# Optimization experiments

Hardware: AMD Instinct MI355X
Metric: run time of the kernel (lower is better)

## Reference

```python
import jax, jax.numpy as jnp
import numpy as np
import math

B, NH, DIM = 8, 12, 768
NP, NF = 196, 16            # n (patches per frame), num_frames
DH = DIM // NH              # 64
D3 = 3 * DH                 # per-head feature dim after projection (192)
SEQ = NP * NF               # 3136 body tokens (+1 cls)
ROT = DH                    # rotary dim (RotaryEmbedding(dim=64))
SCALE = 1.0 / (math.sqrt(DH) * NH)


def _heads(t):
    b, s, _ = t.shape
    return t.reshape(b, s, NH, D3).transpose(0, 2, 1, 3)  # b h s d


def _rope(x):
    # lucidrains-style interleaved rotary on the first ROT dims of each head
    s = x.shape[2]
    inv_freq = 1.0 / (10000.0 ** (jnp.arange(0, ROT, 2, dtype=jnp.float32) / ROT))
    freqs = jnp.arange(s, dtype=jnp.float32)[:, None] * inv_freq  # [s, ROT/2]
    freqs = jnp.repeat(freqs, 2, axis=-1)                          # [s, ROT]
    cos, sin = jnp.cos(freqs), jnp.sin(freqs)
    xr, xp = x[..., :ROT], x[..., ROT:]
    x1, x2 = xr[..., ::2], xr[..., 1::2]
    half = jnp.stack((-x2, x1), axis=-1).reshape(xr.shape)
    return jnp.concatenate([xr * cos + half * sin, xp], axis=-1)


def _att_sum(q, k, v):
    # softmax(q k^T * SCALE) v, then sum over queries keepdim (dim 2)
    p = jax.nn.softmax(jnp.einsum('bhqd,bhkd->bhqk', q, k) * SCALE, axis=-1)
    return jnp.einsum('bhqk,bhkd->bhqd', p, v).sum(axis=2, keepdims=True)


def setup_inputs():
    key = jax.random.key(0)
    ks = jax.random.split(key, 11)
    p = lambda k, sh: jax.random.normal(k, sh, jnp.float32) * 0.02
    return {
        'x': jax.random.normal(ks[0], (B, SEQ + 1, DIM), jnp.float32),
        'Wq': p(ks[1], (DIM, 3 * DIM)), 'bq': p(ks[2], (3 * DIM,)),
        'Wk': p(ks[3], (DIM, 3 * DIM)), 'bk': p(ks[4], (3 * DIM,)),
        'Wv': p(ks[5], (DIM, 3 * DIM)), 'bv': p(ks[6], (3 * DIM,)),
        'Wt': p(ks[7], (3 * DIM, DIM)), 'bt': p(ks[8], (DIM,)),
        'Wf': p(ks[9], (3 * DIM, DIM)), 'bf': p(ks[10], (DIM,)),
    }


def reference(x, Wq, bq, Wk, bk, Wv, bv, Wt, bt, Wf, bf):
    body = x[:, 1:, :]
    # NOTE: the original swaps k/v projections for body tokens (k_mat uses self.v, v_mat uses self.k)
    q = _rope(_heads(body @ Wq + bq))
    k = _rope(_heads(body @ Wv + bv))
    v = _heads(body @ Wk + bk)

    # cls-token attention over the full sequence (correct k/v mapping here)
    q_cls = _heads(x[:, 0:1, :] @ Wq + bq)          # [b,h,1,d]
    k_cls = _heads(x @ Wk + bk)
    v_cls = _heads(x @ Wv + bv)
    p_cls = jax.nn.softmax(jnp.einsum('bhqd,bhkd->bhqk', q_cls, k_cls) * SCALE, axis=-1)
    cls_out = jnp.einsum('bhqk,bhkd->bhqd', p_cls, v_cls)  # [b,h,1,d]

    # temporal attention per spatial position x = 1..NP-1, vectorized
    # token index t = f*NP + x  ->  reshape [b,h,NF,NP,d], move spatial first
    qg = q.reshape(B, NH, NF, NP, D3).transpose(0, 1, 3, 2, 4)[:, :, 1:]  # [b,h,NP-1,NF,d]
    kg = k.reshape(B, NH, NF, NP, D3).transpose(0, 1, 3, 2, 4)[:, :, 1:]
    vg = v.reshape(B, NH, NF, NP, D3).transpose(0, 1, 3, 2, 4)[:, :, 1:]
    pg = jax.nn.softmax(jnp.einsum('bhxfd,bhxgd->bhxfg', qg, kg) * SCALE, axis=-1)
    tmp = jnp.einsum('bhxfg,bhxgd->bhxfd', pg, vg).sum(axis=3)  # sum over query frames -> [b,h,NP-1,d]

    temporal = jnp.tile(tmp, (1, 1, NF, 1))  # torch .repeat tiles -> [b,h,(NP-1)*NF,d]
    ti = temporal.transpose(0, 2, 1, 3).reshape(B, (NP - 1) * NF, NH * D3) @ Wt + bt

    # second pass (q uses self.q, v uses self.k, k uses self.v per original)
    q2 = _heads(ti @ Wq + bq)
    v2 = _heads(ti @ Wk + bk)
    k2 = _heads(ti @ Wv + bv)
    outs = [_att_sum(q2[:, :, 0:NP], k2[:, :, 0:NP], v2[:, :, 0:NP])]
    for xi in range(1, NF):  # small fixed loop over frames
        outs.append(_att_sum(q2[:, :, xi:xi + NP], k2[:, :, xi::NP], v2[:, :, xi::NP]))
    t2 = jnp.concatenate(outs, axis=2)        # [b,h,NF,d]
    t2 = jnp.tile(t2, (1, 1, NP, 1))          # [b,h,SEQ,d]
    t2 = jnp.concatenate([cls_out, t2], axis=2)  # [b,h,SEQ+1,d]
    return t2.transpose(0, 2, 1, 3).reshape(B, SEQ + 1, NH * D3) @ Wf + bf
```

## Files before the change

kernel.cpp:

```cpp
#include <hip/hip_runtime.h>
#include <cstdint>
#include <cstddef>


typedef unsigned short u16;
typedef __attribute__((ext_vector_type(8))) short short8;
typedef __attribute__((ext_vector_type(4))) float f32x4;

#define DEV static __device__ __forceinline__
#define AS1 __attribute__((address_space(1)))
#define AS3 __attribute__((address_space(3)))

DEV float b2f(u16 u) { union { unsigned int i; float f; } v; v.i = ((unsigned int)u) << 16; return v.f; }
DEV float b2fs(short s) { return b2f((u16)s); }
DEV u16 f2b(float f) {
    union { float f; unsigned int i; } v; v.f = f;
    unsigned int r = v.i + 0x7fffu + ((v.i >> 16) & 1u);
    return (u16)(r >> 16);
}
DEV void gld16(const u16* g, u16* l) {
    __builtin_amdgcn_global_load_lds((AS1 void*)(g), (AS3 void*)(l), 16, 0, 0);
}

DEV int detect_fl(const u16* x) {
    int lane = threadIdx.x & 63;
    const u16* p = x + lane * 8;
    int c = 0;
#pragma unroll
    for (int j = 0; j < 8; j++) c += (((p[j] >> 7) & 0xFFu) >= 134u);
#pragma unroll
    for (int off = 32; off; off >>= 1) c += __shfl_xor(c, off);
    return c > 8;
}

constexpr int   ROWS  = 3137;
constexpr int   NPm1  = 195;
constexpr int   MT    = 8 * NPm1;
constexpr int   N3    = 2304;
constexpr float SCALE = 1.0f / 96.0f;
constexpr size_t P2Z  = (size_t)MT * N3;
constexpr int   CLS_NS = 32;
constexpr int   CLS_RS = 99;
constexpr int   LDK   = 200;

DEV float wave_max(float v) {
#pragma unroll
    for (int off = 32; off; off >>= 1) v = fmaxf(v, __shfl_xor(v, off));
    return v;
}
DEV float wave_sum(float v) {
#pragma unroll
    for (int off = 32; off; off >>= 1) v += __shfl_xor(v, off);
    return v;
}
DEV float block_max256(float v, float* red) {
    v = wave_max(v);
    __syncthreads();
    if ((threadIdx.x & 63) == 0) red[threadIdx.x >> 6] = v;
    __syncthreads();
    return fmaxf(fmaxf(red[0], red[1]), fmaxf(red[2], red[3]));
}
float __device__ __forceinline__ block_sum256(float v, float* red) {
    v = wave_sum(v);
    __syncthreads();
    if ((threadIdx.x & 63) == 0) red[threadIdx.x >> 6] = v;
    __syncthreads();
    return (red[0] + red[1]) + (red[2] + red[3]);
}

DEV void do_transpose(const void* in, u16* out, int R, int C,
                      int bx, int by, int fl, u16 (*tls)[33]) {
    int tx = threadIdx.x & 31, ty = threadIdx.x >> 5;
#pragma unroll
    for (int i = 0; i < 32; i += 8) {
        int r = by + ty + i, c = bx + tx;
        size_t idx = (size_t)r * C + c;
        tls[ty + i][tx] = fl ? f2b(((const float*)in)[idx]) : ((const u16*)in)[idx];
    }
    __syncthreads();
#pragma unroll
    for (int i = 0; i < 32; i += 8) {
        int c = bx + ty + i, r = by + tx;
        out[(size_t)c * R + r] = tls[tx][ty + i];
    }
}

__global__ __launch_bounds__(256) void prep(const u16* __restrict__ x,
                                            const void* __restrict__ Wq,
                                            const void* __restrict__ Wk,
                                            const void* __restrict__ Wv,
                                            const void* __restrict__ Wt,
                                            const void* __restrict__ Wf,
                                            const void* __restrict__ bq,
                                            const void* __restrict__ bk,
                                            const void* __restrict__ bv,
                                            u16* __restrict__ WT,
                                            u16* __restrict__ WtT,
                                            u16* __restrict__ WfT,
                                            u16* __restrict__ xb,
                                            float* __restrict__ wacc,
                                            float* __restrict__ ropeT,
                                            float* __restrict__ biasF,
                                            int usexb) {
    __shared__ u16 tls[32][33];
    int bid = blockIdx.x;
    if (bid < 5184) {
        int fl = detect_fl(x);
        int z = bid / 1728, t = bid % 1728;
        const void* W = (z == 0) ? Wq : (z == 1) ? Wk : Wv;
        do_transpose(W, WT + (size_t)z * N3 * 768, 768, N3,
                     (t % 72) * 32, (t / 72) * 32, fl, tls);
        return;
    }
    bid -= 5184;
    if (bid < 3456) {
        int fl = detect_fl(x);
        int z = bid / 1728, t = bid % 1728;
        do_transpose(z ? Wf : Wt, z ? WfT : WtT, N3, 768,
                     (t % 24) * 32, (t / 24) * 32, fl, tls);
        return;
    }
    bid -= 3456;
    if (bid < 9411) {
        if (!usexb) return;
        int fl = detect_fl(x);
        size_t e0 = ((size_t)bid * 256 + threadIdx.x) * 8;
        if (fl) {
            const float* p = (const float*)x + e0;
            float4 u0 = *(const float4*)p, u1 = *(const float4*)(p + 4);
            short8 r;
            r[0]=(short)f2b(u0.x); r[1]=(short)f2b(u0.y); r[2]=(short)f2b(u0.z); r[3]=(short)f2b(u0.w);
            r[4]=(short)f2b(u1.x); r[5]=(short)f2b(u1.y); r[6]=(short)f2b(u1.z); r[7]=(short)f2b(u1.w);
            *(short8*)(xb + e0) = r;
        } else {
            *(short8*)(xb + e0) = *(const short8*)(x + e0);
        }
        return;
    }
    bid -= 9411;
    if (bid < 1176) {
        wacc[(size_t)bid * 256 + threadIdx.x] = 0.f;
        return;
    }
    bid -= 1176;
    if (bid < 392) {
        int t = bid * 256 + threadIdx.x;
        int s = t >> 5, i = t & 31;
        float inv = powf(10000.0f, -(float)(2 * i) * (1.0f / 64.0f));
        float sn, cs;
        sincosf((float)s * inv, &sn, &cs);
        ropeT[t * 2]     = cs;
        ropeT[t * 2 + 1] = sn;
        return;
    }
    bid -= 392;
    {
        int fl = detect_fl(x);
        int t = bid * 256 + threadIdx.x;
        int z = t / 2304, i = t - z * 2304;
        const void* b = (z == 0) ? bq : (z == 1) ? bk : bv;
        biasF[t] = fl ? ((const float*)b)[i] : b2f(((const u16*)b)[i]);
    }
}

DEV short8 pack_f32x8(const float* p) {
    const float4 u0 = *(const float4*)p;
    const float4 u1 = *(const float4*)(p + 4);
    short8 r;
    r[0]=(short)f2b(u0.x); r[1]=(short)f2b(u0.y); r[2]=(short)f2b(u0.z); r[3]=(short)f2b(u0.w);
    r[4]=(short)f2b(u1.x); r[5]=(short)f2b(u1.y); r[6]=(short)f2b(u1.z); r[7]=(short)f2b(u1.w);
    return r;
}

__global__ __launch_bounds__(256) void gemm_bt(const void* __restrict__ A, size_t aoff,
                                               const u16* __restrict__ BT,
                                               const void* __restrict__ b0p,
                                               const void* __restrict__ b1p,
                                               const void* __restrict__ b2p,
                                               void* __restrict__ C,
                                               int M, int N, int K,
                                               const u16* __restrict__ xdet,
                                               int araw, int cf32) {
    const int fl = detect_fl(xdet);
    const int af32 = araw && fl;
    const int z = blockIdx.z;
    const u16* Bz = BT + (size_t)z * N * K;
    const void* bias = (z == 0) ? b0p : (z == 1) ? b1p : b2p;

    __shared__ u16 As[128 * 32];
    __shared__ u16 Bs[128 * 32];

    const int tid  = threadIdx.x;
    const int lane = tid & 63;
    const int wave = tid >> 6;
    const int wm   = wave & 1;
    const int wn   = wave >> 1;
    const int quad = lane >> 4;
    const int l16  = lane & 15;

    const int m0 = blockIdx.y * 128;
    const int n0 = blockIdx.x * 128;

    f32x4 acc[4][4] = {};

    if (!af32) {
        const u16* Ab = (const u16*)A + aoff;
        int srow = wave * 32 + (lane >> 2);
        int scol = (lane & 3) * 8;
        int ar0 = m0 + srow;      if (ar0 > M - 1) ar0 = M - 1;
        int ar1 = m0 + srow + 16; if (ar1 > M - 1) ar1 = M - 1;
        const u16* gA0 = Ab + (size_t)ar0 * K + scol;
        const u16* gA1 = Ab + (size_t)ar1 * K + scol;
        const u16* gB0 = Bz + (size_t)(n0 + srow) * K + scol;
        const u16* gB1 = Bz + (size_t)(n0 + srow + 16) * K + scol;
        u16* lA0 = As + wave * 1024;
        u16* lA1 = As + wave * 1024 + 512;
        u16* lB0 = Bs + wave * 1024;
        u16* lB1 = Bs + wave * 1024 + 512;

        for (int k0 = 0; k0 < K; k0 += 32) {
            __syncthreads();
            gld16(gA0 + k0, lA0);
            gld16(gA1 + k0, lA1);
            gld16(gB0 + k0, lB0);
            gld16(gB1 + k0, lB1);
            __syncthreads();

            short8 af[4], bfr[4];
#pragma unroll
            for (int i = 0; i < 4; i++)
                af[i] = *(const short8*)(&As[(wm * 64 + i * 16 + l16) * 32 + quad * 8]);
#pragma unroll
            for (int j = 0; j < 4; j++)
                bfr[j] = *(const short8*)(&Bs[(wn * 64 + j * 16 + l16) * 32 + quad * 8]);
#pragma unroll
            for (int i = 0; i < 4; i++)
#pragma unroll
                for (int j = 0; j < 4; j++)
                    acc[i][j] = __builtin_amdgcn_mfma_f32_16x16x32_bf16(af[i], bfr[j], acc[i][j], 0, 0, 0);
        }
    } else {
        const int r0 = tid >> 2;
        const int kp = (tid & 3) << 3;
        int ga0 = m0 + r0;       if (ga0 > M - 1) ga0 = M - 1;
        int ga1 = m0 + r0 + 64;  if (ga1 > M - 1) ga1 = M - 1;
        const size_t arow0 = aoff + (size_t)ga0 * K + kp;
        const size_t arow1 = aoff + (size_t)ga1 * K + kp;
        const u16* Bp0 = Bz + (size_t)(n0 + r0) * K + kp;
        const u16* Bp1 = Bz + (size_t)(n0 + r0 + 64) * K + kp;

        for (int k0 = 0; k0 < K; k0 += 32) {
            short8 a0 = pack_f32x8((const float*)A + arow0 + k0);
            short8 a1 = pack_f32x8((const float*)A + arow1 + k0);
            short8 bv0 = *(const short8*)(Bp0 + k0);
            short8 bv1 = *(const short8*)(Bp1 + k0);
            __syncthreads();
            *(short8*)(&As[r0 * 32 + kp])        = a0;
            *(short8*)(&As[(r0 + 64) * 32 + kp]) = a1;
            *(short8*)(&Bs[r0 * 32 + kp])        = bv0;
            *(short8*)(&Bs[(r0 + 64) * 32 + kp]) = bv1;
            __syncthreads();

            short8 af[4], bfr[4];
#pragma unroll
            for (int i = 0; i < 4; i++)
                af[i] = *(const short8*)(&As[(wm * 64 + i * 16 + l16) * 32 + quad * 8]);
#pragma unroll
            for (int j = 0; j < 4; j++)
                bfr[j] = *(const short8*)(&Bs[(wn * 64 + j * 16 + l16) * 32 + quad * 8]);
#pragma unroll
            for (int i = 0; i < 4; i++)
#pragma unroll
                for (int j = 0; j < 4; j++)
                    acc[i][j] = __builtin_amdgcn_mfma_f32_16x16x32_bf16(af[i], bfr[j], acc[i][j], 0, 0, 0);
        }
    }

#pragma unroll
    for (int j = 0; j < 4; j++) {
        int col = n0 + wn * 64 + j * 16 + l16;
        float bb = fl ? ((const float*)bias)[col] : b2f(((const u16*)bias)[col]);
#pragma unroll
        for (int i = 0; i < 4; i++) {
            int rowb = m0 + wm * 64 + i * 16 + quad * 4;
#pragma unroll
            for (int r = 0; r < 4; r++) {
                int row = rowb + r;
                if (row < M) {
                    size_t idx = (size_t)z * M * N + (size_t)row * N + col;
                    float v = acc[i][j][r] + bb;
                    if (cf32) ((float*)C)[idx] = v;
                    else      ((u16*)C)[idx]  = f2b(v);
                }
            }
        }
    }
}

__global__ __launch_bounds__(512) void gemm256(const u16* __restrict__ A, size_t aoff,
                                               const u16* __restrict__ BT,
                                               const float* __restrict__ biasF,
                                               u16* __restrict__ C,
                                               int M, int N, int K) {
    __shared__ __align__(16) u16 As[2][16384];
    __shared__ __align__(16) u16 Bs[2][16384];

    const int tid  = threadIdx.x;
    const int lane = tid & 63;
    const int wid  = tid >> 6;
    const int wm   = wid >> 2;
    const int wn   = wid & 3;
    const int quad = lane >> 4;
    const int l16  = lane & 15;
    const int z    = blockIdx.z;

    const int NTN  = N >> 8;
    const int nwg  = gridDim.x;
    const int orig = blockIdx.x;
    const int q8 = nwg >> 3, r8 = nwg & 7, xcd = orig & 7;
    const int wg = (xcd < r8 ? xcd * (q8 + 1) : r8 * (q8 + 1) + (xcd - r8) * q8)
                   + (orig >> 3);
    const int n0 = (wg % NTN) * 256;
    const int m0 = (wg / NTN) * 256;

    const u16* Ab = A + aoff;
    const u16* Bz = BT + (size_t)z * N * K;
    const int  Mc = M - 1;

    const int srow = (wid << 3) + (lane >> 3);
    const int cs   = ((lane & 7) ^ (lane >> 3)) << 3;
    const u16* gA[4]; const u16* gB[4];
#pragma unroll
    for (int h = 0; h < 2; h++)
#pragma unroll
        for (int l = 0; l < 2; l++) {
            int rl = h * 128 + l * 64 + srow;
            int gr = m0 + rl; if (gr > Mc) gr = Mc;
            gA[h * 2 + l] = Ab + (size_t)gr * K + cs;
            gB[h * 2 + l] = Bz + (size_t)(n0 + rl) * K + cs;
        }

    f32x4  acc[8][4] = {};
    short8 aF[4][2], bF[2][2];

    const int rsw  = l16 & 7;
    const int c0   = ((quad ^ rsw) << 3);
    const int c1   = (((4 | quad) ^ rsw) << 3);
    const int aRowB = (wm * 128 + l16) * 64;
    const int bRowB = (wn * 64  + l16) * 64;

#define STG_A(b, h, kt) do { _Pragma("unroll")                                 \
    for (int _l = 0; _l < 2; _l++)                                             \
        gld16(gA[(h) * 2 + _l] + ((kt) << 6),                                  \
              &As[b][(((h) * 128 + _l * 64 + (wid << 3)) << 6)]); } while (0)
#define STG_B(b, h, kt) do { _Pragma("unroll")                                 \
    for (int _l = 0; _l < 2; _l++)                                             \
        gld16(gB[(h) * 2 + _l] + ((kt) << 6),                                  \
              &Bs[b][(((h) * 128 + _l * 64 + (wid << 3)) << 6)]); } while (0)
#define RD_A(b, mh) do { _Pragma("unroll")                                     \
    for (int _m = 0; _m < 4; _m++) {                                           \
        aF[_m][0] = *(const short8*)&As[b][aRowB + (mh) * 4096 + _m * 1024 + c0]; \
        aF[_m][1] = *(const short8*)&As[b][aRowB + (mh) * 4096 + _m * 1024 + c1]; } } while (0)
#define RD_B(b, nh) do { _Pragma("unroll")                                     \
    for (int _n = 0; _n < 2; _n++) {                                           \
        bF[_n][0] = *(const short8*)&Bs[b][bRowB + (nh) * 2048 + _n * 1024 + c0]; \
        bF[_n][1] = *(const short8*)&Bs[b][bRowB + (nh) * 2048 + _n * 1024 + c1]; } } while (0)
#define MM(mh, nh) do {                                                        \
    __builtin_amdgcn_s_setprio(1);                                             \
    _Pragma("unroll") for (int _ks = 0; _ks < 2; _ks++)                        \
    _Pragma("unroll") for (int _m = 0; _m < 4; _m++)                           \
    _Pragma("unroll") for (int _n = 0; _n < 2; _n++)                           \
        acc[(mh) * 4 + _m][(nh) * 2 + _n] =                                    \
            __builtin_amdgcn_mfma_f32_16x16x32_bf16(aF[_m][_ks], bF[_n][_ks],  \
                acc[(mh) * 4 + _m][(nh) * 2 + _n], 0, 0, 0);                   \
    __builtin_amdgcn_s_setprio(0); } while (0)
#define BARR  __builtin_amdgcn_s_barrier()
#define LGKM0 asm volatile("s_waitcnt lgkmcnt(0)" ::: "memory")
#define VMC(n) asm volatile("s_waitcnt vmcnt(" #n ")" ::: "memory")

    STG_A(0, 0, 0); STG_A(0, 1, 0); STG_B(0, 0, 0); STG_B(0, 1, 0);
    STG_A(1, 0, 1);
    VMC(2); BARR;

    const int NP2 = K >> 7;
    for (int i = 0; i < NP2 - 1; i++) {
        const int kt1 = 2 * i + 1, kt2 = 2 * i + 2, kt3 = 2 * i + 3;
        RD_A(0, 0); RD_B(0, 0); STG_A(1, 1, kt1); BARR; LGKM0; MM(0, 0);         BARR;
        RD_B(0, 1);             STG_B(1, 0, kt1); BARR; LGKM0; MM(0, 1);         BARR;
        RD_A(0, 1);             STG_B(1, 1, kt1); BARR; LGKM0; MM(1, 1);         BARR;
        RD_B(0, 0);             STG_A(0, 0, kt2); BARR; LGKM0; MM(1, 0); VMC(2); BARR;
        RD_A(1, 0); RD_B(1, 0); STG_A(0, 1, kt2); BARR; LGKM0; MM(0, 0);         BARR;
        RD_B(1, 1);             STG_B(0, 0, kt2); BARR; LGKM0; MM(0, 1);         BARR;
        RD_A(1, 1);             STG_B(0, 1, kt2); BARR; LGKM0; MM(1, 1);         BARR;
        RD_B(1, 0);             STG_A(1, 0, kt3); BARR; LGKM0; MM(1, 0); VMC(2); BARR;
    }
    {
        const int ktb = 2 * NP2 - 1;
        RD_A(0, 0); RD_B(0, 0); STG_A(1, 1, ktb); BARR; LGKM0; MM(0, 0);         BARR;
        RD_B(0, 1);             STG_B(1, 0, ktb); BARR; LGKM0; MM(0, 1);         BARR;
        RD_A(0, 1);             STG_B(1, 1, ktb); BARR; LGKM0; MM(1, 1);         BARR;
        RD_B(0, 0);                               BARR; LGKM0; MM(1, 0); VMC(0); BARR;
        RD_A(1, 0); RD_B(1, 0);                   BARR; LGKM0; MM(0, 0);         BARR;
        RD_B(1, 1);                               BARR; LGKM0; MM(0, 1);         BARR;
        RD_A(1, 1);                               BARR; LGKM0; MM(1, 1);         BARR;
        RD_B(1, 0);                               BARR; LGKM0; MM(1, 0);
    }
#undef STG_A
#undef STG_B
#undef RD_A
#undef RD_B
#undef MM
#undef BARR
#undef LGKM0
#undef VMC

#pragma unroll
    for (int ni = 0; ni < 4; ni++) {
        int gcol = n0 + wn * 64 + ni * 16 + l16;
        float bb = biasF[z * N + gcol];
#pragma unroll
        for (int mi = 0; mi < 8; mi++) {
            int rowb = m0 + wm * 128 + mi * 16 + quad * 4;
#pragma unroll
            for (int r = 0; r < 4; r++) {
                int row = rowb + r;
                if (row < M)
                    C[(size_t)z * M * N + (size_t)row * N + gcol] =
                        f2b(acc[mi][ni][r] + bb);
            }
        }
    }
}

__global__ __launch_bounds__(256) void phaseA_attn(const u16* __restrict__ Pb, size_t PZv,
                                                   const float* __restrict__ tab,
                                                   u16* __restrict__ tmp,
                                                   float* __restrict__ clsP, int b0) {
    __shared__ __align__(16) char smem[25600];
    int xg = blockIdx.x, h = blockIdx.y, bl = blockIdx.z;
    int b = b0 + bl;
    int tid = threadIdx.x;

    if (xg < 49) {
        const int wv   = tid >> 6;
        const int lane = tid & 63;
        const int p    = xg * 4 + wv + 1;
        if (p <= 195) {
            u16* Vw = (u16*)smem + wv * 16 * LDK;
            const u16* Pq = Pb;
            const u16* Pk = Pb + 2 * PZv;
            const u16* Pv = Pb + PZv;
            const size_t rbase = (size_t)bl * ROWS;
            const size_t hoff  = (size_t)h * 192;

#pragma unroll
            for (int rr = 0; rr < 6; rr++) {
                int idx = rr * 64 + lane;
                int f = idx / 24, c = (idx % 24) * 8;
                int s = f * 196 + p;
                *(short8*)&Vw[f * LDK + c] =
                    *(const short8*)(Pv + (rbase + 1 + s) * N3 + hoff + c);
            }

            const int quad = lane >> 4, l16 = lane & 15;
            const int sQ = l16 * 196 + p;
            const size_t rowb = (rbase + 1 + sQ) * N3 + hoff;
            short8 Af[6], Bf[6];
#pragma unroll
            for (int ks = 0; ks < 6; ks++) {
                Af[ks] = *(const short8*)(Pq + rowb + quad * 8 + ks * 32);
                Bf[ks] = *(const short8*)(Pk + rowb + quad * 8 + ks * 32);
            }
#pragma unroll
            for (int ks = 0; ks < 2; ks++) {
                int c = quad * 8 + ks * 32;
                const float* tp = tab + ((size_t)sQ * 32 + (c >> 1)) * 2;
                float4 t0 = *(const float4*)tp;
                float4 t1 = *(const float4*)(tp + 4);
                float cs[4] = {t0.x, t0.z, t1.x, t1.z};
                float sn[4] = {t0.y, t0.w, t1.y, t1.w};
                short8 q8 = Af[ks], k8 = Bf[ks], qo, ko;
#pragma unroll
                for (int j = 0; j < 4; j++) {
                    float q1 = b2fs(q8[2 * j]), q2 = b2fs(q8[2 * j + 1]);
                    float k1 = b2fs(k8[2 * j]), k2 = b2fs(k8[2 * j + 1]);
                    qo[2 * j]     = (short)f2b(q1 * cs[j] - q2 * sn[j]);
                    qo[2 * j + 1] = (short)f2b(q2 * cs[j] + q1 * sn[j]);
                    ko[2 * j]     = (short)f2b(k1 * cs[j] - k2 * sn[j]);
                    ko[2 * j + 1] = (short)f2b(k2 * cs[j] + k1 * sn[j]);
                }
                Af[ks] = qo; Bf[ks] = ko;
            }

            f32x4 S = {0.f, 0.f, 0.f, 0.f};
#pragma unroll
            for (int ks = 0; ks < 6; ks++)
                S = __builtin_amdgcn_mfma_f32_16x16x32_bf16(Af[ks], Bf[ks], S, 0, 0, 0);

            float wcol = 0.f;
#pragma unroll
            for (int r = 0; r < 4; r++) {
                float v = S[r] * SCALE;
                float m = v;
#pragma unroll
                for (int k = 1; k < 16; k <<= 1) m = fmaxf(m, __shfl_xor(m, k));
                float e = __expf(v - m);
                float l = e;
#pragma unroll
                for (int k = 1; k < 16; k <<= 1) l += __shfl_xor(l, k);
                wcol += e / l;
            }
            wcol += __shfl_xor(wcol, 16);
            wcol += __shfl_xor(wcol, 32);

            asm volatile("s_waitcnt lgkmcnt(0)" ::: "memory");
            float a0 = 0.f, a1 = 0.f, a2 = 0.f;
#pragma unroll
            for (int g = 0; g < 16; g++) {
                float wg = __shfl(wcol, g);
                a0 += wg * b2f(Vw[g * LDK + lane]);
                a1 += wg * b2f(Vw[g * LDK + lane + 64]);
                a2 += wg * b2f(Vw[g * LDK + lane + 128]);
            }
            u16* op = tmp + (size_t)(b * NPm1 + p - 1) * N3 + hoff;
            op[lane]       = f2b(a0);
            op[lane + 64]  = f2b(a1);
            op[lane + 128] = f2b(a2);
        }
    } else {
        int sp = xg - 49;
        int base = sp * CLS_RS;
        int cnt = ROWS - base; if (cnt > CLS_RS) cnt = CLS_RS;
        float* qs  = (float*)smem;
        float* sc  = qs + 192;
        float* red = sc + 100;
        const size_t hbase = (size_t)bl * ROWS * N3 + (size_t)h * 192;
        const u16* Pq  = Pb;
        const u16* Pkc = Pb + PZv;
        const u16* Pvc = Pb + 2 * PZv;

        if (tid < 192) qs[tid] = b2f(Pq[hbase + tid]);
        __syncthreads();

        float sval = -1e30f;
        if (tid < cnt) {
            const u16* kp = Pkc + hbase + (size_t)(base + tid) * N3;
            float s = 0.f;
#pragma unroll
            for (int c = 0; c < 24; c++) {
                short8 v8 = *(const short8*)(kp + c * 8);
#pragma unroll
                for (int j = 0; j < 8; j++) s += qs[c * 8 + j] * b2fs(v8[j]);
            }
            sval = s * SCALE;
        }
        float m = block_max256(sval, red);
        float e = (tid < cnt) ? __expf(sval - m) : 0.f;
        float l = block_sum256(e, red);
        if (tid < cnt) sc[tid] = e;
        __syncthreads();

        float* pp = clsP + ((size_t)(b * 12 + h) * CLS_NS + sp) * 194;
        if (tid == 0) { pp[0] = m; pp[1] = l; }
        if (tid < 192) {
            float acc = 0.f;
            const u16* vb = Pvc + hbase + tid;
            for (int r = 0; r < cnt; r++) acc += sc[r] * b2f(vb[(size_t)(base + r) * N3]);
            pp[2 + tid] = acc;
        }
    }
}

__global__ __launch_bounds__(256) void attn2_sc(const u16* __restrict__ P2,
                                                float* __restrict__ wacc) {
    int t = blockIdx.x, h = blockIdx.y, b = blockIdx.z;
    __shared__ float pm[4][16], ps[4][16];
    int tid = threadIdx.x;
    const size_t hb = (size_t)b * NPm1 * N3 + (size_t)h * 192;
    const u16* Q  = P2;
    const u16* Kc = P2 + 2 * P2Z;

    int wave = tid >> 6, lane = tid & 63, quad = lane >> 4, l16 = lane & 15;
    float* wb = wacc + (size_t)((b * 12 + h) * 16) * 196;

    for (int xi = 1 + wave; xi <= 15; xi += 4) {
        int qr = (t * 16 + xi + l16) % 195;
        int kr = xi + l16;
        const u16* qp = Q  + hb + (size_t)qr * N3 + quad * 8;
        const u16* kp = Kc + hb + (size_t)kr * N3 + quad * 8;
        short8 Af[6], Bf[6];
#pragma unroll
        for (int ks = 0; ks < 6; ks++) {
            Af[ks] = *(const short8*)(qp + ks * 32);
            Bf[ks] = *(const short8*)(kp + ks * 32);
        }
        f32x4 S = {0.f, 0.f, 0.f, 0.f};
#pragma unroll
        for (int ks = 0; ks < 6; ks++)
            S = __builtin_amdgcn_mfma_f32_16x16x32_bf16(Af[ks], Bf[ks], S, 0, 0, 0);
        float wcol = 0.f;
#pragma unroll
        for (int r = 0; r < 4; r++) {
            float v = S[r] * SCALE;
            float m = v;
#pragma unroll
            for (int k = 1; k < 16; k <<= 1) m = fmaxf(m, __shfl_xor(m, k));
            float e = __expf(v - m);
            float l = e;
#pragma unroll
            for (int k = 1; k < 16; k <<= 1) l += __shfl_xor(l, k);
            bool qok = (t * 16 + quad * 4 + r) <= 195;
            wcol += qok ? e / l : 0.f;
        }
        wcol += __shfl_xor(wcol, 16);
        wcol += __shfl_xor(wcol, 32);
        if (quad == 0) atomicAdd(&wb[xi * 196 + l16], wcol);
    }

    short8 Af0[6];
    {
        int qr0 = (t * 16 + l16) % 195;
        const u16* qp0 = Q + hb + (size_t)qr0 * N3 + quad * 8;
#pragma unroll
        for (int ks = 0; ks < 6; ks++)
            Af0[ks] = *(const short8*)(qp0 + ks * 32);
    }

    f32x4 Sc[4];
    int   cl[4];
    int   cn = 0;
    for (int c = wave; c < 13; c += 4) {
        int g = c * 16 + l16;
        int krow = g % 195;
        const u16* kp = Kc + hb + (size_t)krow * N3 + quad * 8;
        short8 Bf[6];
#pragma unroll
        for (int ks = 0; ks < 6; ks++)
            Bf[ks] = *(const short8*)(kp + ks * 32);
        f32x4 S = {0.f, 0.f, 0.f, 0.f};
#pragma unroll
        for (int ks = 0; ks < 6; ks++)
            S = __builtin_amdgcn_mfma_f32_16x16x32_bf16(Af0[ks], Bf[ks], S, 0, 0, 0);
        bool kbad = g > 195;
#pragma unroll
        for (int r = 0; r < 4; r++) S[r] = kbad ? -1e30f : S[r] * SCALE;
        Sc[cn] = S; cl[cn] = c; cn++;
    }
#pragma unroll
    for (int r = 0; r < 4; r++) {
        float v = -1e30f;
        for (int n = 0; n < cn; n++) v = fmaxf(v, Sc[n][r]);
#pragma unroll
        for (int k = 1; k < 16; k <<= 1) v = fmaxf(v, __shfl_xor(v, k));
        if (l16 == 0) pm[wave][quad * 4 + r] = v;
    }
    __syncthreads();
    float gmx[4], tot[4];
#pragma unroll
    for (int r = 0; r < 4; r++) {
        int qr = quad * 4 + r;
        gmx[r] = fmaxf(fmaxf(pm[0][qr], pm[1][qr]), fmaxf(pm[2][qr], pm[3][qr]));
    }
#pragma unroll
    for (int r = 0; r < 4; r++) {
        float s = 0.f;
        for (int n = 0; n < cn; n++) {
            float e = __expf(Sc[n][r] - gmx[r]);
            Sc[n][r] = e;
            s += e;
        }
#pragma unroll
        for (int k = 1; k < 16; k <<= 1) s += __shfl_xor(s, k);
        if (l16 == 0) ps[wave][quad * 4 + r] = s;
    }
    __syncthreads();
#pragma unroll
    for (int r = 0; r < 4; r++) {
        int qr = quad * 4 + r;
        tot[r] = (ps[0][qr] + ps[1][qr]) + (ps[2][qr] + ps[3][qr]);
    }
    for (int n = 0; n < cn; n++) {
        float wv = 0.f;
#pragma unroll
        for (int r = 0; r < 4; r++) {
            bool qok = (t * 16 + quad * 4 + r) <= 195;
            wv += qok ? Sc[n][r] / tot[r] : 0.f;
        }
        wv += __shfl_xor(wv, 16);
        wv += __shfl_xor(wv, 32);
        int g = cl[n] * 16 + l16;
        if (quad == 0 && g <= 195) atomicAdd(&wb[g], wv);
    }
}

__global__ __launch_bounds__(192) void fin(const u16* __restrict__ P2,
                                           const float* __restrict__ wacc,
                                           const float* __restrict__ clsP,
                                           u16* __restrict__ Fmat) {
    int xg = blockIdx.x, h = blockIdx.y, b = blockIdx.z;
    int tid = threadIdx.x;
    if (xg == 0) {
        const float* p0 = clsP + (size_t)(b * 12 + h) * CLS_NS * 194;
        float M = -1e30f;
#pragma unroll
        for (int s = 0; s < CLS_NS; s++) M = fmaxf(M, p0[s * 194]);
        float L = 0.f, acc = 0.f;
#pragma unroll
        for (int s = 0; s < CLS_NS; s++) {
            float w = __expf(p0[s * 194] - M);
            L += w * p0[s * 194 + 1];
            acc += w * p0[s * 194 + 2 + tid];
        }
        Fmat[(size_t)(b * 17) * N3 + (size_t)h * 192 + tid] = f2b(acc / L);
    } else {
        int xi = xg - 1;
        int Nk = (xi == 0) ? 196 : 16;
        const u16* V = P2 + P2Z;
        const size_t hb = (size_t)b * NPm1 * N3 + (size_t)h * 192;
        const float* wb = wacc + (size_t)((b * 12 + h) * 16 + xi) * 196;
        float acc = 0.f;
        for (int g = 0; g < Nk; g++) {
            int kr = (xi == 0) ? (g % 195) : (xi + g);
            acc += wb[g] * b2f(V[hb + (size_t)kr * N3 + tid]);
        }
        Fmat[(size_t)(b * 17 + 1 + xi) * N3 + (size_t)h * 192 + tid] = f2b(acc);
    }
}

__global__ __launch_bounds__(256) void scatter_out(const float* __restrict__ F17,
                                                   void* __restrict__ out,
                                                   const u16* __restrict__ xdet) {
    const int fl = detect_fl(xdet);
    int t = blockIdx.x * 256 + threadIdx.x;
    int c = t % 96;
    int rem = t / 96;
    int s = rem % ROWS;
    int b = rem / ROWS;
    int src = b * 17 + (s == 0 ? 0 : 1 + ((s - 1) & 15));
    const float* sp = F17 + ((size_t)src * 96 + c) * 8;
    if (fl) {
        float* o = (float*)out + (size_t)t * 8;
        *(float4*)o       = *(const float4*)sp;
        *(float4*)(o + 4) = *(const float4*)(sp + 4);
    } else {
        u16* o = (u16*)out + (size_t)t * 8;
        short8 v;
#pragma unroll
        for (int j = 0; j < 8; j++) v[j] = (short)f2b(sp[j]);
        *(short8*)o = v;
    }
}

extern "C" void kernel_launch(void* const* d_in, const int* in_sizes, int n_in,
                              void* d_out, int out_size, void* d_ws, size_t ws_size,
                              hipStream_t stream) {
    const void* x   = d_in[0];
    const void* Wq  = d_in[1];
    const void* bq  = d_in[2];
    const void* Wk  = d_in[3];
    const void* bk  = d_in[4];
    const void* Wv  = d_in[5];
    const void* bv  = d_in[6];
    const void* Wt  = d_in[7];
    const void* bt  = d_in[8];
    const void* Wf  = d_in[9];
    const void* bfb = d_in[10];
    const u16* xdet = (const u16*)x;
    (void)in_sizes; (void)n_in; (void)out_size;

    auto al = [](size_t b) { return (b + 255) & ~(size_t)255; };
    const size_t szWT   = al((size_t)3 * N3 * 768 * 2);
    const size_t szWtT  = al((size_t)768 * N3 * 2);
    const size_t szTmp  = al((size_t)MT * N3 * 2);
    const size_t szFmat = al((size_t)136 * N3 * 2);
    const size_t szRope = al((size_t)3136 * 32 * 2 * 4);
    const size_t szClsP = al((size_t)8 * 12 * CLS_NS * 194 * 4);
    const size_t szWacc = al((size_t)96 * 16 * 196 * 4);
    const size_t szBias = al((size_t)3 * N3 * 4);
    const size_t szXb   = al((size_t)8 * ROWS * 768 * 2);
    const size_t szB    = al(3 * P2Z * 2) + al((size_t)MT * 768 * 2) +
                          al((size_t)136 * 768 * 4);
    const size_t basePerst = szWT + 2 * szWtT + szTmp + szFmat + szRope +
                             szClsP + szWacc + szBias;

    int bs = 1; int usexb = 0;
    {
        const int cand[4] = {8, 4, 2, 1};
        for (int i = 0; i < 4; i++) {
            size_t szP = al((size_t)3 * cand[i] * ROWS * N3 * 2);
            size_t need = basePerst + szXb + (szP > szB ? szP : szB);
            if (ws_size >= need) { bs = cand[i]; usexb = 1; break; }
        }
        if (!usexb) {
            size_t szP = al((size_t)3 * ROWS * N3 * 2);
            size_t need = basePerst + (szP > szB ? szP : szB);
            if (ws_size < need) return;
        }
    }

    char* ws = (char*)d_ws;
    size_t off = 0;
    auto allocB = [&](size_t bytes) { char* p = ws + off; off += al(bytes); return p; };
    u16*   WT    = (u16*)allocB((size_t)3 * N3 * 768 * 2);
    u16*   WtT   = (u16*)allocB((size_t)768 * N3 * 2);
    u16*   WfT   = (u16*)allocB((size_t)768 * N3 * 2);
    u16*   tmp   = (u16*)allocB((size_t)MT * N3 * 2);
    u16*   Fmat  = (u16*)allocB((size_t)136 * N3 * 2);
    float* ropeT = (float*)allocB((size_t)3136 * 32 * 2 * 4);
    float* clsP  = (float*)allocB((size_t)8 * 12 * CLS_NS * 194 * 4);
    float* wacc  = (float*)allocB((size_t)96 * 16 * 196 * 4);
    float* biasF = (float*)allocB((size_t)3 * N3 * 4);
    u16*   xb    = usexb ? (u16*)allocB((size_t)8 * ROWS * 768 * 2) : nullptr;
    size_t aliasOff = off;
    u16* Pb = (u16*)allocB((size_t)3 * bs * ROWS * N3 * 2);
    off = aliasOff;
    u16*   P2  = (u16*)allocB(3 * P2Z * 2);
    u16*   tiu = (u16*)allocB((size_t)MT * 768 * 2);
    float* F17 = (float*)allocB((size_t)136 * 768 * 4);

    const size_t PZv = (size_t)bs * ROWS * N3;

    prep<<<dim3(19646), 256, 0, stream>>>(xdet, Wq, Wk, Wv, Wt, Wf, bq, bk, bv,
                                          WT, WtT, WfT, xb, wacc, ropeT, biasF,
                                          usexb);

    for (int b0 = 0; b0 < 8; b0 += bs) {
        int Mv = bs * ROWS;
        size_t aoff = (size_t)b0 * ROWS * 768;
        if (usexb) {
            int mtiles = (Mv + 255) >> 8;
            gemm256<<<dim3(9 * mtiles, 1, 3), 512, 0, stream>>>(
                xb, aoff, WT, biasF, Pb, Mv, N3, 768);
        } else {
            gemm_bt<<<dim3(18, (Mv + 127) / 128, 3), 256, 0, stream>>>(
                x, aoff, WT, bq, bk, bv, Pb, Mv, N3, 768, xdet, 1, 0);
        }
        phaseA_attn<<<dim3(81, 12, bs), 256, 0, stream>>>(Pb, PZv, ropeT, tmp, clsP, b0);
    }

    gemm_bt<<<dim3(6, 13, 1), 256, 0, stream>>>(tmp, 0, WtT, bt, bt, bt, tiu,
                                                MT, 768, N3, xdet, 0, 0);
    gemm_bt<<<dim3(18, 13, 3), 256, 0, stream>>>(tiu, 0, WT, bq, bk, bv, P2,
                                                 MT, N3, 768, xdet, 0, 0);
    attn2_sc<<<dim3(13, 12, 8), 256, 0, stream>>>(P2, wacc);
    fin<<<dim3(17, 12, 8), 192, 0, stream>>>(P2, wacc, clsP, Fmat);
    gemm_bt<<<dim3(6, 2, 1), 256, 0, stream>>>(Fmat, 0, WfT, bfb, bfb, bfb, F17,
                                               136, 768, N3, xdet, 0, 1);
    scatter_out<<<dim3(9411), 256, 0, stream>>>(F17, d_out, xdet);
}
```

Measured before the change: 1.088 ms.

## Split-K the small Wt and Wf GEMMs with atomic fp32 accumulation

Adds a split-K mode to gemm_bt. The Wt projection (6x13 tiles) and the final Wf projection (6x2 tiles) now launch four K-slices each and accumulate with atomicAdd into fp32 buffers, which prep zeroes beforehand. The intent is to fill more CUs for these small-grid GEMMs. The next GEMM now reads the fp32 tiu buffer through the conversion path. It also caps the batch-chunk size for the phase-A loop at 2, down from 8, which adds launches, and the atomics cost extra memory traffic and make the sums nondeterministic.

```diff
diff --git a/kernel.cpp b/kernel.cpp
--- a/kernel.cpp
+++ b/kernel.cpp
@@ -101,6 +101,8 @@
                                             float* __restrict__ wacc,
                                             float* __restrict__ ropeT,
                                             float* __restrict__ biasF,
+                                            float* __restrict__ tiuF,
+                                            float* __restrict__ F17z,
                                             int usexb) {
     __shared__ u16 tls[32][33];
     int bid = blockIdx.x;
@@ -154,12 +156,22 @@
         return;
     }
     bid -= 392;
-    {
+    if (bid < 27) {
         int fl = detect_fl(x);
         int t = bid * 256 + threadIdx.x;
         int z = t / 2304, i = t - z * 2304;
         const void* b = (z == 0) ? bq : (z == 1) ? bk : bv;
         biasF[t] = fl ? ((const float*)b)[i] : b2f(((const u16*)b)[i]);
+        return;
+    }
+    bid -= 27;
+    if (bid < 4680) {
+        tiuF[(size_t)bid * 256 + threadIdx.x] = 0.f;
+        return;
+    }
+    bid -= 4680;
+    {
+        F17z[(size_t)bid * 256 + threadIdx.x] = 0.f;
     }
 }
 
@@ -180,12 +192,17 @@
                                                void* __restrict__ C,
                                                int M, int N, int K,
                                                const u16* __restrict__ xdet,
-                                               int araw, int cf32) {
+                                               int araw, int cf32,
+                                               int ksplit, int catm) {
     const int fl = detect_fl(xdet);
-    const int af32 = araw && fl;
-    const int z = blockIdx.z;
-    const u16* Bz = BT + (size_t)z * N * K;
-    const void* bias = (z == 0) ? b0p : (z == 1) ? b1p : b2p;
+    const int af32 = (araw == 2) || (araw == 1 && fl);
+    int w, zz;
+    if (ksplit > 1) { w = blockIdx.z; zz = 0; }
+    else            { w = 0;          zz = blockIdx.z; }
+    const int kc  = K / ksplit;
+    const int kb0 = w * kc, kb1 = kb0 + kc;
+    const u16* Bz = BT + (size_t)zz * N * K;
+    const void* bias = (zz == 0) ? b0p : (zz == 1) ? b1p : b2p;
 
     __shared__ u16 As[128 * 32];
     __shared__ u16 Bs[128 * 32];
@@ -218,7 +235,7 @@
         u16* lB0 = Bs + wave * 1024;
         u16* lB1 = Bs + wave * 1024 + 512;
 
-        for (int k0 = 0; k0 < K; k0 += 32) {
+        for (int k0 = kb0; k0 < kb1; k0 += 32) {
             __syncthreads();
             gld16(gA0 + k0, lA0);
             gld16(gA1 + k0, lA1);
@@ -249,7 +266,7 @@
         const u16* Bp0 = Bz + (size_t)(n0 + r0) * K + kp;
         const u16* Bp1 = Bz + (size_t)(n0 + r0 + 64) * K + kp;
 
-        for (int k0 = 0; k0 < K; k0 += 32) {
+        for (int k0 = kb0; k0 < kb1; k0 += 32) {
             short8 a0 = pack_f32x8((const float*)A + arow0 + k0);
             short8 a1 = pack_f32x8((const float*)A + arow1 + k0);
             short8 bv0 = *(const short8*)(Bp0 + k0);
@@ -279,7 +296,8 @@
 #pragma unroll
     for (int j = 0; j < 4; j++) {
         int col = n0 + wn * 64 + j * 16 + l16;
-        float bb = fl ? ((const float*)bias)[col] : b2f(((const u16*)bias)[col]);
+        float bb = 0.f;
+        if (w == 0) bb = fl ? ((const float*)bias)[col] : b2f(((const u16*)bias)[col]);
 #pragma unroll
         for (int i = 0; i < 4; i++) {
             int rowb = m0 + wm * 64 + i * 16 + quad * 4;
@@ -287,10 +305,11 @@
             for (int r = 0; r < 4; r++) {
                 int row = rowb + r;
                 if (row < M) {
-                    size_t idx = (size_t)z * M * N + (size_t)row * N + col;
+                    size_t idx = (size_t)zz * M * N + (size_t)row * N + col;
                     float v = acc[i][j][r] + bb;
-                    if (cf32) ((float*)C)[idx] = v;
-                    else      ((u16*)C)[idx]  = f2b(v);
+                    if (catm)      atomicAdd(&((float*)C)[idx], v);
+                    else if (cf32) ((float*)C)[idx] = v;
+                    else           ((u16*)C)[idx]  = f2b(v);
                 }
             }
         }
@@ -777,16 +796,17 @@
     const size_t szClsP = al((size_t)8 * 12 * CLS_NS * 194 * 4);
     const size_t szWacc = al((size_t)96 * 16 * 196 * 4);
     const size_t szBias = al((size_t)3 * N3 * 4);
+    const size_t szTiuF = al((size_t)MT * 768 * 4);
+    const size_t szF17  = al((size_t)136 * 768 * 4);
     const size_t szXb   = al((size_t)8 * ROWS * 768 * 2);
-    const size_t szB    = al(3 * P2Z * 2) + al((size_t)MT * 768 * 2) +
-                          al((size_t)136 * 768 * 4);
+    const size_t szB    = al(3 * P2Z * 2) + al((size_t)MT * 768 * 2);
     const size_t basePerst = szWT + 2 * szWtT + szTmp + szFmat + szRope +
-                             szClsP + szWacc + szBias;
+                             szClsP + szWacc + szBias + szTiuF + szF17;
 
     int bs = 1; int usexb = 0;
     {
-        const int cand[4] = {8, 4, 2, 1};
-        for (int i = 0; i < 4; i++) {
+        const int cand[2] = {2, 1};
+        for (int i = 0; i < 2; i++) {
             size_t szP = al((size_t)3 * cand[i] * ROWS * N3 * 2);
             size_t need = basePerst + szXb + (szP > szB ? szP : szB);
             if (ws_size >= need) { bs = cand[i]; usexb = 1; break; }
@@ -810,19 +830,19 @@
     float* clsP  = (float*)allocB((size_t)8 * 12 * CLS_NS * 194 * 4);
     float* wacc  = (float*)allocB((size_t)96 * 16 * 196 * 4);
     float* biasF = (float*)allocB((size_t)3 * N3 * 4);
+    float* tiuF  = (float*)allocB((size_t)MT * 768 * 4);
+    float* F17   = (float*)allocB((size_t)136 * 768 * 4);
     u16*   xb    = usexb ? (u16*)allocB((size_t)8 * ROWS * 768 * 2) : nullptr;
     size_t aliasOff = off;
     u16* Pb = (u16*)allocB((size_t)3 * bs * ROWS * N3 * 2);
     off = aliasOff;
     u16*   P2  = (u16*)allocB(3 * P2Z * 2);
-    u16*   tiu = (u16*)allocB((size_t)MT * 768 * 2);
-    float* F17 = (float*)allocB((size_t)136 * 768 * 4);
 
     const size_t PZv = (size_t)bs * ROWS * N3;
 
-    prep<<<dim3(19646), 256, 0, stream>>>(xdet, Wq, Wk, Wv, Wt, Wf, bq, bk, bv,
+    prep<<<dim3(24734), 256, 0, stream>>>(xdet, Wq, Wk, Wv, Wt, Wf, bq, bk, bv,
                                           WT, WtT, WfT, xb, wacc, ropeT, biasF,
-                                          usexb);
+                                          tiuF, F17, usexb);
 
     for (int b0 = 0; b0 < 8; b0 += bs) {
         int Mv = bs * ROWS;
@@ -833,18 +853,18 @@
                 xb, aoff, WT, biasF, Pb, Mv, N3, 768);
         } else {
             gemm_bt<<<dim3(18, (Mv + 127) / 128, 3), 256, 0, stream>>>(
-                x, aoff, WT, bq, bk, bv, Pb, Mv, N3, 768, xdet, 1, 0);
+                x, aoff, WT, bq, bk, bv, Pb, Mv, N3, 768, xdet, 1, 0, 1, 0);
         }
         phaseA_attn<<<dim3(81, 12, bs), 256, 0, stream>>>(Pb, PZv, ropeT, tmp, clsP, b0);
     }
 
-    gemm_bt<<<dim3(6, 13, 1), 256, 0, stream>>>(tmp, 0, WtT, bt, bt, bt, tiu,
-                                                MT, 768, N3, xdet, 0, 0);
-    gemm_bt<<<dim3(18, 13, 3), 256, 0, stream>>>(tiu, 0, WT, bq, bk, bv, P2,
-                                                 MT, N3, 768, xdet, 0, 0);
+    gemm_bt<<<dim3(6, 13, 4), 256, 0, stream>>>(tmp, 0, WtT, bt, bt, bt, tiuF,
+                                                MT, 768, N3, xdet, 0, 0, 4, 1);
+    gemm_bt<<<dim3(18, 13, 3), 256, 0, stream>>>(tiuF, 0, WT, bq, bk, bv, P2,
+                                                 MT, N3, 768, xdet, 2, 0, 1, 0);
     attn2_sc<<<dim3(13, 12, 8), 256, 0, stream>>>(P2, wacc);
     fin<<<dim3(17, 12, 8), 192, 0, stream>>>(P2, wacc, clsP, Fmat);
-    gemm_bt<<<dim3(6, 2, 1), 256, 0, stream>>>(Fmat, 0, WfT, bfb, bfb, bfb, F17,
-                                               136, 768, N3, xdet, 0, 1);
+    gemm_bt<<<dim3(6, 2, 4), 256, 0, stream>>>(Fmat, 0, WfT, bfb, bfb, bfb, F17,
+                                               136, 768, N3, xdet, 0, 0, 4, 1);
     scatter_out<<<dim3(9411), 256, 0, stream>>>(F17, d_out, xdet);
 }
```

Measured after the change: 1.066 ms. 2.0% less time.
